# Kernel optimization log

Measured on AMD Instinct MI355X. Metric: run time of the kernel, lower is better.

The kernel has to match this reference:

```python
import jax, jax.numpy as jnp
import numpy as np

B, S = 32, 512
VOCAB = 32000
D_MODEL = 512   # embedding dim
HID = 512       # LSTMCell units
LAYERS = 2


def setup_inputs() -> dict:
    key = jax.random.key(0)
    ks = jax.random.split(key, 6)
    source = jax.random.randint(ks[0], (B, S), 0, VOCAB, dtype=jnp.int32)
    source_len = jax.random.randint(ks[1], (B,), 0, S, dtype=jnp.int32)
    emb = jax.random.normal(ks[2], (VOCAB, D_MODEL), dtype=jnp.float32) * 0.02
    # Keras LSTMCell weights: kernel [in_dim, 4*units], recurrent_kernel [units, 4*units],
    # bias [4*units]; gate order i, f, c(g), o. Layer 0 in_dim = D_MODEL == HID here,
    # so all layers stack to one array.
    scale_k = 1.0 / np.sqrt(D_MODEL)
    Wk = jax.random.normal(ks[3], (LAYERS, HID, 4 * HID), dtype=jnp.float32) * scale_k
    Wr = jax.random.normal(ks[4], (LAYERS, HID, 4 * HID), dtype=jnp.float32) * scale_k
    b = jnp.zeros((LAYERS, 4 * HID), dtype=jnp.float32)
    return {"source": source, "source_len": source_len,
            "emb": emb, "Wk": Wk, "Wr": Wr, "b": b}


def _stacked_lstm(x, Wk, Wr, b):
    # x: [B, S, D]; returns [B, S, HID]
    L = Wk.shape[0]
    Bd = x.shape[0]
    h0 = jnp.zeros((L, Bd, HID), dtype=x.dtype)
    c0 = jnp.zeros((L, Bd, HID), dtype=x.dtype)

    def step(carry, x_t):
        h, c = carry            # [L, B, HID]
        inp = x_t               # [B, D]
        hs, cs = [], []
        for l in range(L):
            z = inp @ Wk[l] + h[l] @ Wr[l] + b[l]   # [B, 4*HID]
            i_g, f_g, g_g, o_g = jnp.split(z, 4, axis=-1)
            i_g = jax.nn.sigmoid(i_g)
            f_g = jax.nn.sigmoid(f_g)
            g_g = jnp.tanh(g_g)
            o_g = jax.nn.sigmoid(o_g)
            c_new = f_g * c[l] + i_g * g_g
            h_new = o_g * jnp.tanh(c_new)
            hs.append(h_new)
            cs.append(c_new)
            inp = h_new
        return (jnp.stack(hs), jnp.stack(cs)), inp

    _, ys = jax.lax.scan(step, (h0, c0), jnp.swapaxes(x, 0, 1))  # ys: [S, B, HID]
    return jnp.swapaxes(ys, 0, 1)


def reference(source, source_len, emb, Wk, Wr, b):
    source_emb = emb[source]                    # [B, S, D_MODEL]
    output = _stacked_lstm(source_emb, Wk, Wr, b)  # [B, S, HID]
    return (output, source_emb)
```

## Files before the change

### kernel.cpp

```cpp
#include <hip/hip_runtime.h>
#include <hip/hip_bf16.h>
#include <cstddef>
#include <cstdint>

#define NB 32
#define NS 512
#define ND 512
#define NG 2048

#define FLAGS_OFF 0
#define H1_OFF    4096
#define H1_SLOTS  16
#define H0_OFF    (H1_OFF + H1_SLOTS * 32768)
#define H0_SLOTS  32
#define WS_NEED   (H0_OFF + H0_SLOTS * 32768)

#define POISON   0xFFFFFFFFu
#define SPIN_LIM (1 << 17)

typedef __attribute__((ext_vector_type(8))) short short8;
typedef __attribute__((ext_vector_type(8))) __bf16 bf16x8;
typedef __attribute__((ext_vector_type(4))) float f32x4;

static __device__ __forceinline__ unsigned short f2bf(float f) {
  __hip_bfloat16 h = __float2bfloat16(f);
  return __builtin_bit_cast(unsigned short, h);
}

static __device__ __forceinline__ short8 pack8(float4 a, float4 b) {
  short8 r;
  r[0] = (short)f2bf(a.x); r[1] = (short)f2bf(a.y);
  r[2] = (short)f2bf(a.z); r[3] = (short)f2bf(a.w);
  r[4] = (short)f2bf(b.x); r[5] = (short)f2bf(b.y);
  r[6] = (short)f2bf(b.z); r[7] = (short)f2bf(b.w);
  return r;
}

static __device__ __forceinline__ unsigned long long aload64(const unsigned char* p) {
  return __hip_atomic_load(reinterpret_cast<const unsigned long long*>(p),
                           __ATOMIC_RELAXED, __HIP_MEMORY_SCOPE_AGENT);
}

#define BARRIER_LGKM() asm volatile("s_waitcnt lgkmcnt(0)\n\ts_barrier" ::: "memory")

__global__ __launch_bounds__(256) void gather_f32(const int* __restrict__ src,
                                                  const float* __restrict__ emb,
                                                  float* __restrict__ out1) {
  int tid = blockIdx.x * 256 + threadIdx.x;
  int bt = tid >> 7;
  int k4 = (tid & 127) << 2;
  int s  = src[bt];
  float4 v = *reinterpret_cast<const float4*>(emb + (size_t)s * ND + k4);
  *reinterpret_cast<float4*>(out1 + (size_t)bt * ND + k4) = v;
}

__global__ __launch_bounds__(320, 1) void lstm_persist(
    const float* __restrict__ Wk, const float* __restrict__ Wr,
    const float* __restrict__ bias_g,
    const float* __restrict__ x_f32,
    unsigned char* ws, float* __restrict__ out0) {

  __shared__ __attribute__((aligned(16))) char smem[66048];

  const int tid   = threadIdx.x;
  const int bid   = blockIdx.x;
  const int L     = bid >> 6;
  const int slice = bid & 63;
  const int u0    = slice * 8;
  const int lane  = tid & 63;
  const int wv    = tid >> 6;
  const int m     = wv & 1;
  const int kh    = wv >> 1;

  const float* WkL = Wk + (size_t)L * 512 * NG;
  const float* WrL = Wr + (size_t)L * 512 * NG;

  short* WT = reinterpret_cast<short*>(smem);
  for (int idx = tid; idx < 1024 * 32; idx += 320) {
    int k = idx >> 5, c = idx & 31;
    int gc = (c >> 3) * 512 + u0 + (c & 7);
    float v = (k < 512) ? WkL[(size_t)k * NG + gc]
                        : WrL[(size_t)(k - 512) * NG + gc];
    WT[c * 1032 + k] = (short)f2bf(v);
  }
  __syncthreads();

  short8 Bf[2][16];
  if (wv < 4) {
    int colr = lane & 15;
    int q    = lane >> 4;
#pragma unroll
    for (int n = 0; n < 2; ++n)
#pragma unroll
      for (int kt2 = 0; kt2 < 16; ++kt2) {
        int k = (kh * 16 + kt2) * 32 + q * 8;
        Bf[n][kt2] = *reinterpret_cast<const short8*>(WT + (n * 16 + colr) * 1032 + k);
      }
  }
  __syncthreads();

  float* zb   = reinterpret_cast<float*>(smem);
  float* blds = zb + 2 * 2112;
  if (tid < 32) {
    int gc = (tid >> 3) * 512 + u0 + (tid & 7);
    blds[tid] = bias_g[L * NG + gc];
  }
  __syncthreads();

  int* flags = reinterpret_cast<int*>(ws + FLAGS_OFF);
  unsigned char* h1buf = ws + H1_OFF;
  unsigned char* h0buf = ws + H0_OFF;

  const int eb   = lane >> 1;
  const int eu_b = (lane & 1) * 4;
  const size_t pub_base = (size_t)(eb >> 4) * 16384 + (size_t)(u0 >> 5) * 1024 +
                          (size_t)((u0 >> 3) & 3) * 256 + (size_t)(eb & 15) * 16 +
                          (size_t)eu_b * 2;
  float creg0 = 0.f, creg1 = 0.f, creg2 = 0.f, creg3 = 0.f;

  for (int t = 0; t <= NS; ++t) {
    if (wv < 4 && t < NS) {
      short8 af[16];

      if (L == 0 && kh == 0) {
        int bpf = 0;
        const bool bp = (wv == 0) && ((t & 3) == 0) && (t >= 16);
        if (bp) bpf = (int)__hip_atomic_load(flags + lane, __ATOMIC_RELAXED,
                                             __HIP_MEMORY_SCOPE_AGENT);
        int bb = m * 16 + (lane & 15);
        const float* xr = x_f32 + ((size_t)bb * NS + t) * ND + (lane >> 4) * 8;
#pragma unroll
        for (int kt2 = 0; kt2 < 16; ++kt2) {
          float4 v0 = *reinterpret_cast<const float4*>(xr + kt2 * 32);
          float4 v1 = *reinterpret_cast<const float4*>(xr + kt2 * 32 + 4);
          af[kt2] = pack8(v0, v1);
        }
        if (bp) {
          int sp = 0;
          while (!__all(bpf >= t - 10)) {
            if (++sp > SPIN_LIM) break;
            __builtin_amdgcn_s_sleep(8);
            bpf = (int)__hip_atomic_load(flags + lane, __ATOMIC_RELAXED,
                                         __HIP_MEMORY_SCOPE_AGENT);
          }
        }
      } else if (t == 0 && kh == 1) {
        const short8 zz = {0, 0, 0, 0, 0, 0, 0, 0};
#pragma unroll
        for (int kt2 = 0; kt2 < 16; ++kt2) af[kt2] = zz;
      } else {
        const unsigned char* hb;
        if (L == 0)       hb = h0buf + (size_t)((t - 1) & 31) * 32768;
        else if (kh == 0) hb = h0buf + (size_t)(t & 31) * 32768;
        else              hb = h1buf + (size_t)((t - 1) & 15) * 32768;
        const unsigned char* ha = hb + (size_t)m * 16384 +
                                  (size_t)(lane >> 4) * 256 + (size_t)(lane & 15) * 16;
        int spin = 0;
        for (;;) {
#pragma unroll
          for (int i = 0; i < 4; ++i) {
#pragma unroll
            for (int j = 0; j < 4; ++j) {
              unsigned long long* ap =
                  reinterpret_cast<unsigned long long*>(&af[i * 4 + j]);
              const unsigned char* p = ha + (size_t)i * 4096 + (size_t)j * 1024;
              ap[0] = aload64(p);
              ap[1] = aload64(p + 8);
            }
          }
          unsigned ok = 1u;
#pragma unroll
          for (int i = 0; i < 16; ++i) {
            const unsigned long long* ap =
                reinterpret_cast<const unsigned long long*>(&af[i]);
            unsigned w0 = (unsigned)ap[0], w1 = (unsigned)(ap[0] >> 32);
            unsigned w2 = (unsigned)ap[1], w3 = (unsigned)(ap[1] >> 32);
            ok &= (unsigned)(w0 != POISON) & (unsigned)(w1 != POISON) &
                  (unsigned)(w2 != POISON) & (unsigned)(w3 != POISON);
          }
          if (ok) break;
          if (++spin > SPIN_LIM) break;
          if (spin > 8) __builtin_amdgcn_s_sleep(1);
        }
      }

      f32x4 acc0 = {0.f, 0.f, 0.f, 0.f}, acc1 = {0.f, 0.f, 0.f, 0.f};
#pragma unroll
      for (int kt2 = 0; kt2 < 16; ++kt2) {
        bf16x8 a = __builtin_bit_cast(bf16x8, af[kt2]);
        acc0 = __builtin_amdgcn_mfma_f32_16x16x32_bf16(
            a, __builtin_bit_cast(bf16x8, Bf[0][kt2]), acc0, 0, 0, 0);
        acc1 = __builtin_amdgcn_mfma_f32_16x16x32_bf16(
            a, __builtin_bit_cast(bf16x8, Bf[1][kt2]), acc1, 0, 0, 0);
      }

      {
        int r0 = m * 16 + (lane >> 4) * 4;
        int cc = lane & 15;
        float* zp = zb + (t & 1) * 2112 + kh * (32 * 33);
#pragma unroll
        for (int r = 0; r < 4; ++r) {
          zp[(r0 + r) * 33 + cc]      = acc0[r];
          zp[(r0 + r) * 33 + 16 + cc] = acc1[r];
        }
      }
    } else if (wv == 4 && t > 0) {
      const int tp = t - 1;
      const float* zq = zb + (tp & 1) * 2112;
      float hv0, hv1, hv2, hv3;
      {
        float hv[4];
#pragma unroll
        for (int j = 0; j < 4; ++j) {
          int eu = eu_b + j;
          float zi = zq[eb * 33 + eu]      + zq[1056 + eb * 33 + eu]      + blds[eu];
          float zf = zq[eb * 33 + 8 + eu]  + zq[1056 + eb * 33 + 8 + eu]  + blds[8 + eu];
          float zg = zq[eb * 33 + 16 + eu] + zq[1056 + eb * 33 + 16 + eu] + blds[16 + eu];
          float zo = zq[eb * 33 + 24 + eu] + zq[1056 + eb * 33 + 24 + eu] + blds[24 + eu];
          float ig = 1.f / (1.f + __expf(-zi));
          float fg = 1.f / (1.f + __expf(-zf));
          float e2 = __expf(-2.f * zg);
          float gg = (1.f - e2) / (1.f + e2);
          float og = 1.f / (1.f + __expf(-zo));
          float c_old = (j == 0) ? creg0 : (j == 1) ? creg1 : (j == 2) ? creg2 : creg3;
          float c_new = fg * c_old + ig * gg;
          if (j == 0) creg0 = c_new; else if (j == 1) creg1 = c_new;
          else if (j == 2) creg2 = c_new; else creg3 = c_new;
          float ec = __expf(-2.f * c_new);
          hv[j] = og * ((1.f - ec) / (1.f + ec));
        }
        hv0 = hv[0]; hv1 = hv[1]; hv2 = hv[2]; hv3 = hv[3];
      }

      unsigned p0 = ((unsigned)f2bf(hv0) & 0xffffu) | ((unsigned)f2bf(hv1) << 16);
      unsigned p1 = ((unsigned)f2bf(hv2) & 0xffffu) | ((unsigned)f2bf(hv3) << 16);
      unsigned char* dst = (L == 0)
          ? h0buf + (size_t)(tp & 31) * 32768 + pub_base
          : h1buf + (size_t)(tp & 15) * 32768 + pub_base;
      __hip_atomic_store(reinterpret_cast<unsigned*>(dst), p0,
                         __ATOMIC_RELAXED, __HIP_MEMORY_SCOPE_AGENT);
      __hip_atomic_store(reinterpret_cast<unsigned*>(dst + 4), p1,
                         __ATOMIC_RELAXED, __HIP_MEMORY_SCOPE_AGENT);

      unsigned char* pb = (L == 0)
          ? h0buf + (size_t)((tp + 16) & 31) * 32768 + pub_base
          : h1buf + (size_t)((tp + 8) & 15) * 32768 + pub_base;
      __hip_atomic_store(reinterpret_cast<unsigned*>(pb), POISON,
                         __ATOMIC_RELAXED, __HIP_MEMORY_SCOPE_AGENT);
      __hip_atomic_store(reinterpret_cast<unsigned*>(pb + 4), POISON,
                         __ATOMIC_RELAXED, __HIP_MEMORY_SCOPE_AGENT);

      if (L == 1) {
        float4 o4 = make_float4(hv0, hv1, hv2, hv3);
        *reinterpret_cast<float4*>(
            out0 + ((size_t)eb * NS + tp) * ND + u0 + eu_b) = o4;
        if (lane == 0)
          __hip_atomic_store(flags + slice, tp, __ATOMIC_RELAXED,
                             __HIP_MEMORY_SCOPE_AGENT);
      }
      asm volatile("s_waitcnt vmcnt(8)" ::: "memory");
    }

    BARRIER_LGKM();
  }
}

extern "C" void kernel_launch(void* const* d_in, const int* in_sizes, int n_in,
                              void* d_out, int out_size, void* d_ws, size_t ws_size,
                              hipStream_t stream) {
  const int*   src = (const int*)d_in[0];
  const float* emb = (const float*)d_in[2];
  const float* Wk  = (const float*)d_in[3];
  const float* Wr  = (const float*)d_in[4];
  const float* bg  = (const float*)d_in[5];

  float* out0 = (float*)d_out;
  float* out1 = out0 + (size_t)NB * NS * ND;
  unsigned char* ws = (unsigned char*)d_ws;

  gather_f32<<<8192, 256, 0, stream>>>(src, emb, out1);

  hipMemsetAsync(ws + FLAGS_OFF, 0, H1_OFF, stream);
  hipMemsetAsync(ws + H1_OFF, 0xFF, WS_NEED - H1_OFF, stream);

  lstm_persist<<<128, 320, 0, stream>>>(Wk, Wr, bg, out1, ws, out0);
}
```

Before: 2.830 ms.

## Pin each LSTM layer to one XCD and use XCD-local polling for hidden-state exchange

Launches 512 blocks and has each block read its XCC_ID and claim a role so that all 64 layer-0 blocks and all 64 layer-1 blocks sit on XCD 0 and XCD 1 respectively. When a layer is fully co-located, hidden-state exchange uses non-device-coherent sc0 loads and stores, with a periodic sc0 sc1 reload, which should cut cross-XCD coherence latency on the per-step polling path. With a large enough workspace, layer-0 outputs go to a full 512-slot buffer so layer 1 no longer needs the backpressure flags or poison writes. The cost is the claim handshake, a timeout fallback and extra dual writes for layer 0, and correctness now depends on the assumed XCD placement and cache behaviour.

Result: slower. 3.721 ms (+31.5%).

```diff
diff --git a/kernel.cpp b/kernel.cpp
--- a/kernel.cpp
+++ b/kernel.cpp
@@ -8,12 +8,12 @@
 #define ND 512
 #define NG 2048
 
-#define FLAGS_OFF 0
-#define H1_OFF    4096
-#define H1_SLOTS  16
-#define H0_OFF    (H1_OFF + H1_SLOTS * 32768)
-#define H0_SLOTS  32
-#define WS_NEED   (H0_OFF + H0_SLOTS * 32768)
+#define CLAIM_BYTES 4096
+#define H1_OFF   CLAIM_BYTES
+#define H0F_OFF  (H1_OFF + 16 * 32768)
+#define H0M_OFF  (H0F_OFF + 16 * 32768)
+#define WS_FULL  ((size_t)H0M_OFF + 512ull * 32768ull)
+#define WS_SMALL ((size_t)H0M_OFF + 32ull * 32768ull)
 
 #define POISON   0xFFFFFFFFu
 #define SPIN_LIM (1 << 17)
@@ -21,6 +21,7 @@
 typedef __attribute__((ext_vector_type(8))) short short8;
 typedef __attribute__((ext_vector_type(8))) __bf16 bf16x8;
 typedef __attribute__((ext_vector_type(4))) float f32x4;
+typedef __attribute__((ext_vector_type(4))) unsigned int u32x4;
 
 static __device__ __forceinline__ unsigned short f2bf(float f) {
   __hip_bfloat16 h = __float2bfloat16(f);
@@ -40,8 +41,48 @@
   return __hip_atomic_load(reinterpret_cast<const unsigned long long*>(p),
                            __ATOMIC_RELAXED, __HIP_MEMORY_SCOPE_AGENT);
 }
+static __device__ __forceinline__ int aload_i(const int* p) {
+  return __hip_atomic_load(p, __ATOMIC_RELAXED, __HIP_MEMORY_SCOPE_AGENT);
+}
+static __device__ __forceinline__ int aload_acq(const int* p) {
+  return __hip_atomic_load(p, __ATOMIC_ACQUIRE, __HIP_MEMORY_SCOPE_AGENT);
+}
+static __device__ __forceinline__ void astore_i(int* p, int v) {
+  __hip_atomic_store(p, v, __ATOMIC_RELAXED, __HIP_MEMORY_SCOPE_AGENT);
+}
+static __device__ __forceinline__ void astore_u(unsigned char* p, unsigned v) {
+  __hip_atomic_store(reinterpret_cast<unsigned*>(p), v,
+                     __ATOMIC_RELAXED, __HIP_MEMORY_SCOPE_AGENT);
+}
+static __device__ __forceinline__ int afadd(int* p, int v) {
+  return __hip_atomic_fetch_add(p, v, __ATOMIC_RELAXED, __HIP_MEMORY_SCOPE_AGENT);
+}
+static __device__ __forceinline__ int afadd_rel(int* p, int v) {
+  return __hip_atomic_fetch_add(p, v, __ATOMIC_RELEASE, __HIP_MEMORY_SCOPE_AGENT);
+}
+
+static __device__ __forceinline__ int read_xcc() {
+  int x;
+  asm volatile("s_getreg_b32 %0, hwreg(HW_REG_XCC_ID)" : "=s"(x));
+  return x & 15;
+}
 
 #define BARRIER_LGKM() asm volatile("s_waitcnt lgkmcnt(0)\n\ts_barrier" ::: "memory")
+
+#define LDQ_S(dst, base, off)                                                   \
+  asm volatile("global_load_dwordx4 %0, %1, off offset:" #off " sc0"            \
+               : "=v"(dst) : "v"(base))
+#define LDQ_D(dst, base, off)                                                   \
+  asm volatile("global_load_dwordx4 %0, %1, off offset:" #off " sc0 sc1"        \
+               : "=v"(dst) : "v"(base))
+#define LD16(M)                                                                 \
+  M(af[0],  b0, 0);    M(af[1],  b0, 1024); M(af[2],  b0, 2048); M(af[3],  b0, 3072); \
+  M(af[4],  b1, 0);    M(af[5],  b1, 1024); M(af[6],  b1, 2048); M(af[7],  b1, 3072); \
+  M(af[8],  b2, 0);    M(af[9],  b2, 1024); M(af[10], b2, 2048); M(af[11], b2, 3072); \
+  M(af[12], b3, 0);    M(af[13], b3, 1024); M(af[14], b3, 2048); M(af[15], b3, 3072)
+
+#define STW_S(addr, val)                                                        \
+  asm volatile("global_store_dword %0, %1, off sc0" :: "v"(addr), "v"(val))
 
 __global__ __launch_bounds__(256) void gather_f32(const int* __restrict__ src,
                                                   const float* __restrict__ emb,
@@ -54,6 +95,7 @@
   *reinterpret_cast<float4*>(out1 + (size_t)bt * ND + k4) = v;
 }
 
+template<bool FULL>
 __global__ __launch_bounds__(320, 1) void lstm_persist(
     const float* __restrict__ Wk, const float* __restrict__ Wr,
     const float* __restrict__ bias_g,
@@ -61,16 +103,68 @@
     unsigned char* ws, float* __restrict__ out0) {
 
   __shared__ __attribute__((aligned(16))) char smem[66048];
-
-  const int tid   = threadIdx.x;
-  const int bid   = blockIdx.x;
-  const int L     = bid >> 6;
-  const int slice = bid & 63;
+  __shared__ int s_role, s_fast0, s_fast1;
+
+  const int tid  = threadIdx.x;
+  const int lane = tid & 63;
+  const int wv   = tid >> 6;
+  const int m    = wv & 1;
+  const int kh   = wv >> 1;
+
+  int* cl     = reinterpret_cast<int*>(ws);
+  int* flags  = cl + 32;
+  int* xcdtab = cl + 128;
+
+  if (tid == 0) {
+    int xcd  = read_xcc();
+    int role = -1;
+    if (xcd == 0)      { int v = afadd(cl + 0, 1); if (v < 64) role = v; }
+    else if (xcd == 1) { int v = afadd(cl + 1, 1); if (v < 64) role = 64 + v; }
+    if (role < 0) {
+      unsigned long long t0 = __builtin_amdgcn_s_memrealtime();
+      for (;;) {
+        if (aload_i(cl + 2) >= 128) break;
+        if (__builtin_amdgcn_s_memrealtime() - t0 > 6000ull) {
+          int v = afadd(cl + 0, 1);
+          if (v < 64) { role = v; astore_i(cl + 3, 1); }
+          else {
+            v = afadd(cl + 1, 1);
+            if (v < 64) { role = 64 + v; astore_i(cl + 4, 1); }
+          }
+          break;
+        }
+        __builtin_amdgcn_s_sleep(8);
+      }
+    }
+    if (role >= 0) {
+      astore_i(xcdtab + role, xcd + 1);
+      afadd_rel(cl + 2, 1);
+    }
+    s_role = role;
+  }
+  __syncthreads();
+  const int role = s_role;
+  if (role < 0) return;
+  if (tid == 0) {
+    int sp = 0;
+    while (aload_acq(cl + 2) < 128) {
+      if (++sp > SPIN_LIM) break;
+      __builtin_amdgcn_s_sleep(8);
+    }
+  }
+  __syncthreads();
+  if (wv == 0) {
+    int x0 = aload_i(xcdtab + lane), x1 = aload_i(xcdtab + 64 + lane);
+    int e0 = __all(x0 == __shfl(x0, 0)) && (aload_i(cl + 3) == 0);
+    int e1 = __all(x1 == __shfl(x1, 0)) && (aload_i(cl + 4) == 0);
+    if (lane == 0) { s_fast0 = e0; s_fast1 = e1; }
+  }
+  __syncthreads();
+  const bool fast0 = (s_fast0 != 0), fast1 = (s_fast1 != 0);
+
+  const int L     = role >> 6;
+  const int slice = role & 63;
   const int u0    = slice * 8;
-  const int lane  = tid & 63;
-  const int wv    = tid >> 6;
-  const int m     = wv & 1;
-  const int kh    = wv >> 1;
 
   const float* WkL = Wk + (size_t)L * 512 * NG;
   const float* WrL = Wr + (size_t)L * 512 * NG;
@@ -107,9 +201,9 @@
   }
   __syncthreads();
 
-  int* flags = reinterpret_cast<int*>(ws + FLAGS_OFF);
   unsigned char* h1buf = ws + H1_OFF;
-  unsigned char* h0buf = ws + H0_OFF;
+  unsigned char* h0f   = ws + H0F_OFF;
+  unsigned char* h0m   = ws + H0M_OFF;
 
   const int eb   = lane >> 1;
   const int eu_b = (lane & 1) * 4;
@@ -124,9 +218,8 @@
 
       if (L == 0 && kh == 0) {
         int bpf = 0;
-        const bool bp = (wv == 0) && ((t & 3) == 0) && (t >= 16);
-        if (bp) bpf = (int)__hip_atomic_load(flags + lane, __ATOMIC_RELAXED,
-                                             __HIP_MEMORY_SCOPE_AGENT);
+        const bool bp = (!FULL) && (wv == 0) && ((t & 3) == 0) && (t >= 16);
+        if (bp) bpf = aload_i(flags + lane);
         int bb = m * 16 + (lane & 15);
         const float* xr = x_f32 + ((size_t)bb * NS + t) * ND + (lane >> 4) * 8;
 #pragma unroll
@@ -138,10 +231,9 @@
         if (bp) {
           int sp = 0;
           while (!__all(bpf >= t - 10)) {
-            if (++sp > SPIN_LIM) break;
-            __builtin_amdgcn_s_sleep(8);
-            bpf = (int)__hip_atomic_load(flags + lane, __ATOMIC_RELAXED,
-                                         __HIP_MEMORY_SCOPE_AGENT);
+            if (++sp > 4096) break;
+            __builtin_amdgcn_s_sleep(4);
+            bpf = aload_i(flags + lane);
           }
         }
       } else if (t == 0 && kh == 1) {
@@ -150,37 +242,65 @@
         for (int kt2 = 0; kt2 < 16; ++kt2) af[kt2] = zz;
       } else {
         const unsigned char* hb;
-        if (L == 0)       hb = h0buf + (size_t)((t - 1) & 31) * 32768;
-        else if (kh == 0) hb = h0buf + (size_t)(t & 31) * 32768;
-        else              hb = h1buf + (size_t)((t - 1) & 15) * 32768;
+        bool fp;
+        if (L == 0) {
+          fp = fast0;
+          hb = fp ? h0f + (size_t)((t - 1) & 15) * 32768
+                  : h0m + (size_t)(FULL ? (t - 1) : ((t - 1) & 31)) * 32768;
+        } else if (kh == 0) {
+          fp = false;
+          hb = h0m + (size_t)(FULL ? t : (t & 31)) * 32768;
+        } else {
+          fp = fast1;
+          hb = h1buf + (size_t)((t - 1) & 15) * 32768;
+        }
         const unsigned char* ha = hb + (size_t)m * 16384 +
                                   (size_t)(lane >> 4) * 256 + (size_t)(lane & 15) * 16;
-        int spin = 0;
-        for (;;) {
-#pragma unroll
-          for (int i = 0; i < 4; ++i) {
-#pragma unroll
-            for (int j = 0; j < 4; ++j) {
-              unsigned long long* ap =
-                  reinterpret_cast<unsigned long long*>(&af[i * 4 + j]);
-              const unsigned char* p = ha + (size_t)i * 4096 + (size_t)j * 1024;
-              ap[0] = aload64(p);
-              ap[1] = aload64(p + 8);
+        if (fp) {
+          const unsigned char* b0 = ha;
+          const unsigned char* b1 = ha + 4096;
+          const unsigned char* b2 = ha + 8192;
+          const unsigned char* b3 = ha + 12288;
+          int spin = 0;
+          for (;;) {
+            if ((spin & 15) == 15) { LD16(LDQ_D); } else { LD16(LDQ_S); }
+            asm volatile("s_waitcnt vmcnt(0)" ::: "memory");
+            __builtin_amdgcn_sched_barrier(0);
+            unsigned ok = 1u;
+#pragma unroll
+            for (int i = 0; i < 16; ++i) {
+              u32x4 w = __builtin_bit_cast(u32x4, af[i]);
+              ok &= (unsigned)(w[0] != POISON) & (unsigned)(w[1] != POISON) &
+                    (unsigned)(w[2] != POISON) & (unsigned)(w[3] != POISON);
             }
+            if (ok) break;
+            if (++spin > SPIN_LIM) break;
+            if (spin > 8) __builtin_amdgcn_s_sleep(1);
           }
-          unsigned ok = 1u;
-#pragma unroll
-          for (int i = 0; i < 16; ++i) {
-            const unsigned long long* ap =
-                reinterpret_cast<const unsigned long long*>(&af[i]);
-            unsigned w0 = (unsigned)ap[0], w1 = (unsigned)(ap[0] >> 32);
-            unsigned w2 = (unsigned)ap[1], w3 = (unsigned)(ap[1] >> 32);
-            ok &= (unsigned)(w0 != POISON) & (unsigned)(w1 != POISON) &
-                  (unsigned)(w2 != POISON) & (unsigned)(w3 != POISON);
+        } else {
+          int spin = 0;
+          for (;;) {
+#pragma unroll
+            for (int i = 0; i < 4; ++i)
+#pragma unroll
+              for (int j = 0; j < 4; ++j) {
+                unsigned long long* ap =
+                    reinterpret_cast<unsigned long long*>(&af[i * 4 + j]);
+                const unsigned char* p = ha + (size_t)i * 4096 + (size_t)j * 1024;
+                ap[0] = aload64(p);
+                ap[1] = aload64(p + 8);
+              }
+            unsigned ok = 1u;
+#pragma unroll
+            for (int i = 0; i < 16; ++i) {
+              u32x4 w = __builtin_bit_cast(u32x4, af[i]);
+              ok &= (unsigned)(w[0] != POISON) & (unsigned)(w[1] != POISON) &
+                    (unsigned)(w[2] != POISON) & (unsigned)(w[3] != POISON);
+            }
+            if (ok) break;
+            if (++spin > SPIN_LIM) break;
+            if (spin > 8) __builtin_amdgcn_s_sleep(1);
           }
-          if (ok) break;
-          if (++spin > SPIN_LIM) break;
-          if (spin > 8) __builtin_amdgcn_s_sleep(1);
         }
       }
 
@@ -234,29 +354,34 @@
 
       unsigned p0 = ((unsigned)f2bf(hv0) & 0xffffu) | ((unsigned)f2bf(hv1) << 16);
       unsigned p1 = ((unsigned)f2bf(hv2) & 0xffffu) | ((unsigned)f2bf(hv3) << 16);
-      unsigned char* dst = (L == 0)
-          ? h0buf + (size_t)(tp & 31) * 32768 + pub_base
-          : h1buf + (size_t)(tp & 15) * 32768 + pub_base;
-      __hip_atomic_store(reinterpret_cast<unsigned*>(dst), p0,
-                         __ATOMIC_RELAXED, __HIP_MEMORY_SCOPE_AGENT);
-      __hip_atomic_store(reinterpret_cast<unsigned*>(dst + 4), p1,
-                         __ATOMIC_RELAXED, __HIP_MEMORY_SCOPE_AGENT);
-
-      unsigned char* pb = (L == 0)
-          ? h0buf + (size_t)((tp + 16) & 31) * 32768 + pub_base
-          : h1buf + (size_t)((tp + 8) & 15) * 32768 + pub_base;
-      __hip_atomic_store(reinterpret_cast<unsigned*>(pb), POISON,
-                         __ATOMIC_RELAXED, __HIP_MEMORY_SCOPE_AGENT);
-      __hip_atomic_store(reinterpret_cast<unsigned*>(pb + 4), POISON,
-                         __ATOMIC_RELAXED, __HIP_MEMORY_SCOPE_AGENT);
-
-      if (L == 1) {
+
+      if (L == 0) {
+        unsigned char* dm = h0m + (size_t)(FULL ? tp : (tp & 31)) * 32768 + pub_base;
+        astore_u(dm, p0); astore_u(dm + 4, p1);
+        if (!FULL) {
+          unsigned char* pm = h0m + (size_t)((tp + 16) & 31) * 32768 + pub_base;
+          astore_u(pm, POISON); astore_u(pm + 4, POISON);
+        }
+        if (fast0) {
+          unsigned char* df = h0f + (size_t)(tp & 15) * 32768 + pub_base;
+          unsigned char* pf = h0f + (size_t)((tp + 8) & 15) * 32768 + pub_base;
+          STW_S(df, p0); STW_S(df + 4, p1);
+          STW_S(pf, POISON); STW_S(pf + 4, POISON);
+        }
+      } else {
+        unsigned char* dst = h1buf + (size_t)(tp & 15) * 32768 + pub_base;
+        unsigned char* pb  = h1buf + (size_t)((tp + 8) & 15) * 32768 + pub_base;
+        if (fast1) {
+          STW_S(dst, p0); STW_S(dst + 4, p1);
+          STW_S(pb, POISON); STW_S(pb + 4, POISON);
+        } else {
+          astore_u(dst, p0); astore_u(dst + 4, p1);
+          astore_u(pb, POISON); astore_u(pb + 4, POISON);
+        }
         float4 o4 = make_float4(hv0, hv1, hv2, hv3);
         *reinterpret_cast<float4*>(
             out0 + ((size_t)eb * NS + tp) * ND + u0 + eu_b) = o4;
-        if (lane == 0)
-          __hip_atomic_store(flags + slice, tp, __ATOMIC_RELAXED,
-                             __HIP_MEMORY_SCOPE_AGENT);
+        if (!FULL && lane == 0) astore_i(flags + slice, tp);
       }
       asm volatile("s_waitcnt vmcnt(8)" ::: "memory");
     }
@@ -280,8 +405,12 @@
 
   gather_f32<<<8192, 256, 0, stream>>>(src, emb, out1);
 
-  hipMemsetAsync(ws + FLAGS_OFF, 0, H1_OFF, stream);
-  hipMemsetAsync(ws + H1_OFF, 0xFF, WS_NEED - H1_OFF, stream);
-
-  lstm_persist<<<128, 320, 0, stream>>>(Wk, Wr, bg, out1, ws, out0);
-}
+  bool full = ws_size >= WS_FULL;
+  size_t poison_bytes = (full ? WS_FULL : WS_SMALL) - H1_OFF;
+
+  hipMemsetAsync(ws, 0, CLAIM_BYTES, stream);
+  hipMemsetAsync(ws + H1_OFF, 0xFF, poison_bytes, stream);
+
+  if (full) lstm_persist<true ><<<512, 320, 0, stream>>>(Wk, Wr, bg, out1, ws, out0);
+  else      lstm_persist<false><<<512, 320, 0, stream>>>(Wk, Wr, bg, out1, ws, out0);
+}
```
